# Optimization experiments

Measured on AMD Instinct MI355X. Metric: run time of the kernel, lower is better.

Reference implementation:

```python
import jax, jax.numpy as jnp
import numpy as np

HID, H, D, DFF = 128, 4, 128, 2048   # hidden_dim, nheads, out_feats per head, dim_feedforward
N, E, B = 32768, 524288, 32
EPS = 1e-5
SLOPE = 0.2  # DGL EdgeGATConv negative_slope default


def setup_inputs() -> dict:
    key = jax.random.key(0)
    ks = jax.random.split(key, 16)
    s = 0.05
    return {
        "h": jax.random.normal(ks[0], (N, HID), jnp.float32),
        "e": jax.random.normal(ks[1], (E, 1), jnp.float32),
        "src": jax.random.randint(ks[2], (E,), 0, N, jnp.int32),
        "dst": jax.random.randint(ks[3], (E,), 0, N, jnp.int32),
        "batch_size": B,
        # EdgeGATConv params (fc / fc_edge / res_fc are bias-free in DGL)
        "W_fc": jax.random.normal(ks[4], (HID, H * D), jnp.float32) * s,
        "attn_l": jax.random.normal(ks[5], (H, D), jnp.float32) * s,
        "attn_r": jax.random.normal(ks[6], (H, D), jnp.float32) * s,
        "W_fe": jax.random.normal(ks[7], (1, H * D), jnp.float32) * s,
        "attn_e": jax.random.normal(ks[8], (H, D), jnp.float32) * s,
        "W_res": jax.random.normal(ks[9], (HID, H * D), jnp.float32) * s,
        "gat_bias": jnp.zeros((H * D,), jnp.float32),
        # linear_mha + norms + FFN
        "W_mha": jax.random.normal(ks[10], (H * D, HID), jnp.float32) * s,
        "b_mha": jnp.zeros((HID,), jnp.float32),
        "n1_g": jnp.ones((HID,), jnp.float32),
        "n1_b": jnp.zeros((HID,), jnp.float32),
        "n2_g": jnp.ones((HID,), jnp.float32),
        "n2_b": jnp.zeros((HID,), jnp.float32),
        "W1": jax.random.normal(ks[11], (HID, DFF), jnp.float32) * s,
        "b1": jnp.zeros((DFF,), jnp.float32),
        "W2": jax.random.normal(ks[12], (DFF, HID), jnp.float32) * s,
        "b2": jnp.zeros((HID,), jnp.float32),
    }


def _ln(x, g, b):
    mu = x.mean(-1, keepdims=True)
    var = ((x - mu) ** 2).mean(-1, keepdims=True)
    return (x - mu) * jax.lax.rsqrt(var + EPS) * g + b


def reference(h, e, src, dst, batch_size, W_fc, attn_l, attn_r, W_fe, attn_e,
              W_res, gat_bias, W_mha, b_mha, n1_g, n1_b, n2_g, n2_b,
              W1, b1, W2, b2):
    n = h.shape[0]
    h0 = h
    # --- EdgeGATConv (eval mode: dropouts are identity) ---
    ft = (h @ W_fc).reshape(n, H, D)                         # (N,H,D)
    el = jnp.einsum("nhd,hd->nh", ft, attn_l)                # (N,H)
    er = jnp.einsum("nhd,hd->nh", ft, attn_r)
    fe = (e @ W_fe).reshape(-1, H, D)                        # (E,H,D)
    ee = jnp.einsum("ehd,hd->eh", fe, attn_e)                # (E,H)
    sc = jax.nn.leaky_relu(el[src] + er[dst] + ee, SLOPE)    # (E,H)
    # segment softmax over incoming edges of each dst node
    m = jax.ops.segment_max(sc, dst, num_segments=n)         # (N,H)
    m = jnp.where(jnp.isfinite(m), m, 0.0)                   # empty segments
    w = jnp.exp(sc - m[dst])
    z = jax.ops.segment_sum(w, dst, num_segments=n)
    zd = z[dst]
    alpha = w / jnp.where(zd == 0, 1.0, zd)                  # (E,H)
    msg = ft[src] * alpha[:, :, None]                        # (E,H,D)
    rst = jax.ops.segment_sum(msg, dst, num_segments=n)      # (N,H,D)
    rst = rst + (h0 @ W_res).reshape(n, H, D) + gat_bias.reshape(1, H, D)
    # --- transformer wrapper ---
    x = jax.nn.relu(rst).reshape(n, H * D)
    x = jax.nn.relu(x @ W_mha + b_mha)
    x = _ln(h0 + x, n1_g, n1_b)
    x = x.reshape(batch_size, -1, x.shape[1])                # (B, N/B, HID)
    ff = jax.nn.relu(x @ W1 + b1) @ W2 + b2
    return _ln(x + ff, n2_g, n2_b)
```

## Files before the change

kernel.cpp:

```cpp
#include <hip/hip_runtime.h>
#include <hip/hip_bf16.h>

#define N_NODES 32768
#define E_EDGES 524288
#define HIDDIM 128
#define FDIM 512
#define DFF 2048
#define LN_EPS 1e-5f
#define SLOPE 0.2f
#define CAP 64

typedef __bf16 bf16_t;
typedef __bf16 bf16x8 __attribute__((ext_vector_type(8)));
typedef float f32x4 __attribute__((ext_vector_type(4)));
typedef float f32x2 __attribute__((ext_vector_type(2)));

#define GLD_LDS16(gp, lp) __builtin_amdgcn_global_load_lds( \
    (const __attribute__((address_space(1))) unsigned int*)(gp), \
    (__attribute__((address_space(3))) unsigned int*)(lp), 16, 0, 0)

__device__ inline unsigned char f32_to_e4m3(float v) {
#if __has_builtin(__builtin_amdgcn_cvt_pk_fp8_f32)
    return (unsigned char)(__builtin_amdgcn_cvt_pk_fp8_f32(v, v, 0, false) & 0xff);
#else
    unsigned bits = __float_as_uint(v);
    unsigned sign = (bits >> 24) & 0x80;
    float av = fabsf(v);
    if (av >= 448.f) return (unsigned char)(sign | 0x7E);
    int e = (int)((bits >> 23) & 0xFF) - 127;
    if (e < -6) { int n = (int)rintf(av * 512.f); return (unsigned char)(sign | n); }
    float ulp = exp2f((float)(e - 3));
    int n = (int)rintf(av / ulp);
    if (n == 16) { e += 1; n = 8; }
    return (unsigned char)(sign | ((e + 7) << 3) | (n - 8));
#endif
}
template<bool HI>
__device__ inline f32x2 e4m3x2_to_f32(unsigned u) {
#if __has_builtin(__builtin_amdgcn_cvt_pk_f32_fp8)
    return __builtin_amdgcn_cvt_pk_f32_fp8(u, HI);
#else
    f32x2 r;
    unsigned b0 = HI ? ((u >> 16) & 0xff) : (u & 0xff);
    unsigned b1 = HI ? ((u >> 24) & 0xff) : ((u >> 8) & 0xff);
    unsigned bs[2] = {b0, b1};
    for (int i = 0; i < 2; ++i) {
        unsigned b = bs[i];
        float s = (b & 0x80) ? -1.f : 1.f;
        int e = (b >> 3) & 15, m = b & 7;
        float v = e ? (8 + m) * exp2f((float)(e - 10)) : m * exp2f(-9.f);
        r[i] = s * v;
    }
    return r;
#endif
}

__device__ inline void pack_range(const float* __restrict__ B, bf16_t* __restrict__ out,
                                  int id, int N) {
    const int g = id / N, n = id % N;
    union { bf16_t b[8]; uint4 u; } pk;
#pragma unroll
    for (int j = 0; j < 8; ++j) pk.b[j] = (bf16_t)B[(size_t)(g * 8 + j) * N + n];
    *(uint4*)(out + (size_t)id * 8) = pk.u;
}

__global__ __launch_bounds__(256) void prep_kernel(const float* __restrict__ h, bf16_t* __restrict__ hb,
                                                   const float* __restrict__ W_fc, bf16_t* __restrict__ Wfc_p,
                                                   const float* __restrict__ W_res, bf16_t* __restrict__ Wres_p,
                                                   const float* __restrict__ W_mha, bf16_t* __restrict__ Wmha_p,
                                                   const float* __restrict__ W1, bf16_t* __restrict__ W1_p,
                                                   const float* __restrict__ W2, bf16_t* __restrict__ W2_p,
                                                   const float* __restrict__ W_fe, const float* __restrict__ attn_e,
                                                   float* __restrict__ ce) {
    int bid = blockIdx.x;
    const int tid = threadIdx.x;
    if (bid < 4096) {
        const int id = bid * 256 + tid;
        const float4 v = ((const float4*)h)[id];
        union { bf16_t b[4]; uint2 u; } pk;
        pk.b[0] = (bf16_t)v.x; pk.b[1] = (bf16_t)v.y; pk.b[2] = (bf16_t)v.z; pk.b[3] = (bf16_t)v.w;
        *(uint2*)(hb + (size_t)id * 4) = pk.u;
        return;
    }
    bid -= 4096;
    if (bid < 32)  { pack_range(W_fc,  Wfc_p,  bid * 256 + tid, 512);  return; }
    bid -= 32;
    if (bid < 32)  { pack_range(W_res, Wres_p, bid * 256 + tid, 512);  return; }
    bid -= 32;
    if (bid < 32)  { pack_range(W_mha, Wmha_p, bid * 256 + tid, 128);  return; }
    bid -= 32;
    if (bid < 128) { pack_range(W1,    W1_p,   bid * 256 + tid, 2048); return; }
    bid -= 128;
    if (bid < 128) { pack_range(W2,    W2_p,   bid * 256 + tid, 128);  return; }
    if (tid < 128) {
        const float4 w = ((const float4*)W_fe)[tid];
        const float4 a = ((const float4*)attn_e)[tid];
        float p = w.x * a.x + w.y * a.y + w.z * a.z + w.w * a.w;
        for (int off = 16; off; off >>= 1) p += __shfl_down(p, off, 32);
        if ((tid & 31) == 0) ce[tid >> 5] = p;
    }
}

__global__ __launch_bounds__(256) void gemm_mfma(const bf16_t* __restrict__ A,
                                                 const bf16_t* __restrict__ Bp,
                                                 bf16_t* __restrict__ C,
                                                 int M, int N, int K) {
    __shared__ __align__(16) bf16_t lA[4096];
    __shared__ __align__(16) bf16_t lB[4096];
    const int tid = threadIdx.x;
    const int lane = tid & 63;
    const int wave = tid >> 6;
    const int wm = (wave >> 1) * 64, wn = (wave & 1) * 64;
    const int row0 = blockIdx.y * 128, col0 = blockIdx.x * 128;
    const int ko = lane >> 4;
    const int rl = lane & 15;
    f32x4 acc[4][4] = {};
    const int c0 = tid, c1 = tid + 256;
    const int g0 = c0 >> 7, m0 = c0 & 127;
    const int g1 = c1 >> 7, m1 = c1 & 127;
    for (int k0 = 0; k0 < K; k0 += 32) {
        __syncthreads();
        GLD_LDS16(A + (size_t)(row0 + m0) * K + k0 + g0 * 8, lA + c0 * 8);
        GLD_LDS16(A + (size_t)(row0 + m1) * K + k0 + g1 * 8, lA + c1 * 8);
        GLD_LDS16(Bp + ((size_t)(k0 / 8 + g0) * N + col0 + m0) * 8, lB + c0 * 8);
        GLD_LDS16(Bp + ((size_t)(k0 / 8 + g1) * N + col0 + m1) * 8, lB + c1 * 8);
        __syncthreads();
        bf16x8 af[4], bfr[4];
#pragma unroll
        for (int i = 0; i < 4; ++i) {
            af[i]  = *(const bf16x8*)&lA[(ko * 128 + wm + i * 16 + rl) * 8];
            bfr[i] = *(const bf16x8*)&lB[(ko * 128 + wn + i * 16 + rl) * 8];
        }
#pragma unroll
        for (int i = 0; i < 4; ++i)
#pragma unroll
            for (int j = 0; j < 4; ++j)
                acc[i][j] = __builtin_amdgcn_mfma_f32_16x16x32_bf16(af[i], bfr[j], acc[i][j], 0, 0, 0);
    }
    const int cr = (lane >> 4) * 4;
    const int cc = lane & 15;
#pragma unroll
    for (int i = 0; i < 4; ++i)
#pragma unroll
        for (int j = 0; j < 4; ++j) {
            const int col = col0 + wn + j * 16 + cc;
#pragma unroll
            for (int r = 0; r < 4; ++r) {
                const int row = row0 + wm + i * 16 + cr + r;
                C[(size_t)row * N + col] = (bf16_t)acc[i][j][r];
            }
        }
}

__global__ __launch_bounds__(256) void gemm_ft(const bf16_t* __restrict__ A,
                                               const bf16_t* __restrict__ Bp,
                                               const float* __restrict__ attn_l,
                                               const float* __restrict__ attn_r,
                                               unsigned char* __restrict__ ft8,
                                               float* __restrict__ el,
                                               float* __restrict__ er) {
    __shared__ __align__(16) bf16_t lA[4096];
    __shared__ __align__(16) bf16_t lB[4096];
    __shared__ float s_el[2][128], s_er[2][128];
    const int tid = threadIdx.x, lane = tid & 63, wave = tid >> 6;
    const int wm = (wave >> 1) * 64, wn = (wave & 1) * 64;
    const int row0 = blockIdx.y * 128;
    const int head = blockIdx.x, col0 = head * 128;
    const int ko = lane >> 4, rl = lane & 15;
    f32x4 acc[4][4] = {};
    const int c0 = tid, c1 = tid + 256;
    const int g0 = c0 >> 7, m0 = c0 & 127;
    const int g1 = c1 >> 7, m1 = c1 & 127;
    for (int k0 = 0; k0 < 128; k0 += 32) {
        __syncthreads();
        GLD_LDS16(A + (size_t)(row0 + m0) * 128 + k0 + g0 * 8, lA + c0 * 8);
        GLD_LDS16(A + (size_t)(row0 + m1) * 128 + k0 + g1 * 8, lA + c1 * 8);
        GLD_LDS16(Bp + ((size_t)(k0 / 8 + g0) * 512 + col0 + m0) * 8, lB + c0 * 8);
        GLD_LDS16(Bp + ((size_t)(k0 / 8 + g1) * 512 + col0 + m1) * 8, lB + c1 * 8);
        __syncthreads();
        bf16x8 af[4], bfr[4];
#pragma unroll
        for (int i = 0; i < 4; ++i) {
            af[i]  = *(const bf16x8*)&lA[(ko * 128 + wm + i * 16 + rl) * 8];
            bfr[i] = *(const bf16x8*)&lB[(ko * 128 + wn + i * 16 + rl) * 8];
        }
#pragma unroll
        for (int i = 0; i < 4; ++i)
#pragma unroll
            for (int j = 0; j < 4; ++j)
                acc[i][j] = __builtin_amdgcn_mfma_f32_16x16x32_bf16(af[i], bfr[j], acc[i][j], 0, 0, 0);
    }
    const int cr = (lane >> 4) * 4, cc = lane & 15;
    float al[4], ar[4];
#pragma unroll
    for (int j = 0; j < 4; ++j) {
        al[j] = attn_l[col0 + wn + j * 16 + cc];
        ar[j] = attn_r[col0 + wn + j * 16 + cc];
    }
#pragma unroll
    for (int i = 0; i < 4; ++i)
#pragma unroll
        for (int r = 0; r < 4; ++r) {
            const int row = row0 + wm + i * 16 + cr + r;
            float pel = 0.f, per = 0.f;
#pragma unroll
            for (int j = 0; j < 4; ++j) {
                const float v = acc[i][j][r];
                ft8[(size_t)row * 512 + col0 + wn + j * 16 + cc] = f32_to_e4m3(v);
                pel += v * al[j];
                per += v * ar[j];
            }
#pragma unroll
            for (int m = 1; m < 16; m <<= 1) {
                pel += __shfl_xor(pel, m);
                per += __shfl_xor(per, m);
            }
            if (cc == 0) {
                s_el[wn >> 6][wm + i * 16 + cr + r] = pel;
                s_er[wn >> 6][wm + i * 16 + cr + r] = per;
            }
        }
    __syncthreads();
    if (tid < 128) {
        el[(size_t)(row0 + tid) * 4 + head] = s_el[0][tid] + s_el[1][tid];
        er[(size_t)(row0 + tid) * 4 + head] = s_er[0][tid] + s_er[1][tid];
    }
}

__global__ __launch_bounds__(256) void gemm_mha_ln(const bf16_t* __restrict__ A,
                                                   const bf16_t* __restrict__ Bp,
                                                   const float* __restrict__ bias,
                                                   const float* __restrict__ h0,
                                                   const float* __restrict__ gamma,
                                                   const float* __restrict__ beta,
                                                   bf16_t* __restrict__ out) {
    __shared__ __align__(16) bf16_t lA[4096];
    __shared__ __align__(16) bf16_t lB[4096];
    __shared__ float s_s1[2][128], s_s2[2][128], s_mu[128], s_rs[128];
    const int tid = threadIdx.x, lane = tid & 63, wave = tid >> 6;
    const int wm = (wave >> 1) * 64, wn = (wave & 1) * 64;
    const int row0 = blockIdx.x * 128;
    const int ko = lane >> 4, rl = lane & 15;
    f32x4 acc[4][4] = {};
    const int c0 = tid, c1 = tid + 256;
    const int g0 = c0 >> 7, m0 = c0 & 127;
    const int g1 = c1 >> 7, m1 = c1 & 127;
    for (int k0 = 0; k0 < 512; k0 += 32) {
        __syncthreads();
        GLD_LDS16(A + (size_t)(row0 + m0) * 512 + k0 + g0 * 8, lA + c0 * 8);
        GLD_LDS16(A + (size_t)(row0 + m1) * 512 + k0 + g1 * 8, lA + c1 * 8);
        GLD_LDS16(Bp + ((size_t)(k0 / 8 + g0) * 128 + m0) * 8, lB + c0 * 8);
        GLD_LDS16(Bp + ((size_t)(k0 / 8 + g1) * 128 + m1) * 8, lB + c1 * 8);
        __syncthreads();
        bf16x8 af[4], bfr[4];
#pragma unroll
        for (int i = 0; i < 4; ++i) {
            af[i]  = *(const bf16x8*)&lA[(ko * 128 + wm + i * 16 + rl) * 8];
            bfr[i] = *(const bf16x8*)&lB[(ko * 128 + wn + i * 16 + rl) * 8];
        }
#pragma unroll
        for (int i = 0; i < 4; ++i)
#pragma unroll
            for (int j = 0; j < 4; ++j)
                acc[i][j] = __builtin_amdgcn_mfma_f32_16x16x32_bf16(af[i], bfr[j], acc[i][j], 0, 0, 0);
    }
    const int cr = (lane >> 4) * 4, cc = lane & 15;
#pragma unroll
    for (int j = 0; j < 4; ++j) {
        const int col = wn + j * 16 + cc;
        const float bb = bias[col];
#pragma unroll
        for (int i = 0; i < 4; ++i)
#pragma unroll
            for (int r = 0; r < 4; ++r) {
                const int row = row0 + wm + i * 16 + cr + r;
                acc[i][j][r] = fmaxf(acc[i][j][r] + bb, 0.f) + h0[(size_t)row * 128 + col];
            }
    }
#pragma unroll
    for (int i = 0; i < 4; ++i)
#pragma unroll
        for (int r = 0; r < 4; ++r) {
            float s1 = 0.f, s2 = 0.f;
#pragma unroll
            for (int j = 0; j < 4; ++j) { const float v = acc[i][j][r]; s1 += v; s2 += v * v; }
#pragma unroll
            for (int m = 1; m < 16; m <<= 1) {
                s1 += __shfl_xor(s1, m);
                s2 += __shfl_xor(s2, m);
            }
            if (cc == 0) {
                s_s1[wn >> 6][wm + i * 16 + cr + r] = s1;
                s_s2[wn >> 6][wm + i * 16 + cr + r] = s2;
            }
        }
    __syncthreads();
    if (tid < 128) {
        const float a = s_s1[0][tid] + s_s1[1][tid];
        const float q = s_s2[0][tid] + s_s2[1][tid];
        const float mu = a * (1.f / 128.f);
        s_mu[tid] = mu;
        s_rs[tid] = rsqrtf(q * (1.f / 128.f) - mu * mu + LN_EPS);
    }
    __syncthreads();
#pragma unroll
    for (int j = 0; j < 4; ++j) {
        const int col = wn + j * 16 + cc;
        const float gg = gamma[col], bb = beta[col];
#pragma unroll
        for (int i = 0; i < 4; ++i)
#pragma unroll
            for (int r = 0; r < 4; ++r) {
                const int rloc = wm + i * 16 + cr + r;
                out[(size_t)(row0 + rloc) * 128 + col] =
                    (bf16_t)((acc[i][j][r] - s_mu[rloc]) * s_rs[rloc] * gg + bb);
            }
    }
}

__global__ __launch_bounds__(256, 1) void ffn_fused(const bf16_t* __restrict__ x3,
                                                    const bf16_t* __restrict__ W1p,
                                                    const float* __restrict__ b1,
                                                    const bf16_t* __restrict__ W2p,
                                                    const float* __restrict__ b2,
                                                    const float* __restrict__ gamma,
                                                    const float* __restrict__ beta,
                                                    float* __restrict__ out) {
    __shared__ __align__(16) bf16_t lW1[2][8192];
    __shared__ __align__(16) bf16_t lW2[2][8192];
    __shared__ __align__(16) bf16_t lY[8192];
    const int tid = threadIdx.x, lane = tid & 63, wave = tid >> 6;
    const int wr = wave * 32;
    const int row0 = blockIdx.x * 128;
    const int ko = lane >> 4, rl = lane & 15;
    const int cr = ko * 4, cc = rl;

#pragma unroll
    for (int it = 0; it < 4; ++it) {
        const int c = it * 256 + tid;
        { const int g = c >> 6, n = c & 63;  GLD_LDS16(W1p + ((size_t)g * 2048 + n) * 8, lW1[0] + c * 8); }
        { const int g = c >> 7, n = c & 127; GLD_LDS16(W2p + ((size_t)g * 128 + n) * 8, lW2[0] + c * 8); }
    }
    bf16x8 afx[2][4];
#pragma unroll
    for (int i = 0; i < 2; ++i)
#pragma unroll
        for (int kk = 0; kk < 4; ++kk)
            afx[i][kk] = *(const bf16x8*)&x3[(size_t)(row0 + wr + i * 16 + rl) * 128 + (kk * 4 + ko) * 8];
    __syncthreads();

    f32x4 xacc[2][8] = {};
    for (int ch = 0; ch < 32; ++ch) {
        const int b = ch & 1;
        if (ch + 1 < 32) {
            const int nb = b ^ 1, nch = ch + 1;
#pragma unroll
            for (int it = 0; it < 4; ++it) {
                const int c = it * 256 + tid;
                { const int g = c >> 6, n = c & 63;  GLD_LDS16(W1p + ((size_t)g * 2048 + nch * 64 + n) * 8, lW1[nb] + c * 8); }
                { const int g = c >> 7, n = c & 127; GLD_LDS16(W2p + ((size_t)(nch * 8 + g) * 128 + n) * 8, lW2[nb] + c * 8); }
            }
        }
        f32x4 yacc[2][4] = {};
#pragma unroll
        for (int kk = 0; kk < 4; ++kk) {
            bf16x8 bfr[4];
#pragma unroll
            for (int j = 0; j < 4; ++j)
                bfr[j] = *(const bf16x8*)&lW1[b][((kk * 4 + ko) * 64 + j * 16 + rl) * 8];
#pragma unroll
            for (int i = 0; i < 2; ++i)
#pragma unroll
                for (int j = 0; j < 4; ++j)
                    yacc[i][j] = __builtin_amdgcn_mfma_f32_16x16x32_bf16(afx[i][kk], bfr[j], yacc[i][j], 0, 0, 0);
        }
#pragma unroll
        for (int j = 0; j < 4; ++j) {
            const int dff = j * 16 + cc;
            const float bb = b1[ch * 64 + dff];
#pragma unroll
            for (int i = 0; i < 2; ++i)
#pragma unroll
                for (int r = 0; r < 4; ++r)
                    lY[((dff >> 3) * 128 + wr + i * 16 + cr + r) * 8 + (dff & 7)] =
                        (bf16_t)fmaxf(yacc[i][j][r] + bb, 0.f);
        }
#pragma unroll
        for (int kk = 0; kk < 2; ++kk) {
            bf16x8 afY[2];
#pragma unroll
            for (int i = 0; i < 2; ++i)
                afY[i] = *(const bf16x8*)&lY[((kk * 4 + ko) * 128 + wr + i * 16 + rl) * 8];
#pragma unroll
            for (int j = 0; j < 8; ++j) {
                const bf16x8 bfr2 = *(const bf16x8*)&lW2[b][((kk * 4 + ko) * 128 + j * 16 + rl) * 8];
#pragma unroll
                for (int i = 0; i < 2; ++i)
                    xacc[i][j] = __builtin_amdgcn_mfma_f32_16x16x32_bf16(afY[i], bfr2, xacc[i][j], 0, 0, 0);
            }
        }
        __syncthreads();
    }
#pragma unroll
    for (int i = 0; i < 2; ++i)
#pragma unroll
        for (int r = 0; r < 4; ++r) {
            const int row = wr + i * 16 + cr + r;
            float s1 = 0.f, s2 = 0.f;
#pragma unroll
            for (int j = 0; j < 8; ++j) {
                const int col = j * 16 + cc;
                float v = xacc[i][j][r] + b2[col] + (float)x3[(size_t)(row0 + row) * 128 + col];
                xacc[i][j][r] = v;
                s1 += v; s2 += v * v;
            }
#pragma unroll
            for (int m = 1; m < 16; m <<= 1) {
                s1 += __shfl_xor(s1, m);
                s2 += __shfl_xor(s2, m);
            }
            const float mu = s1 * (1.f / 128.f);
            const float rs = rsqrtf(s2 * (1.f / 128.f) - mu * mu + LN_EPS);
#pragma unroll
            for (int j = 0; j < 8; ++j) {
                const int col = j * 16 + cc;
                out[(size_t)(row0 + row) * 128 + col] =
                    (xacc[i][j][r] - mu) * rs * gamma[col] + beta[col];
            }
        }
}

__global__ __launch_bounds__(256) void edge_build(const float* __restrict__ evals,
                                                  const int* __restrict__ src,
                                                  const int* __restrict__ dst,
                                                  const float* __restrict__ el,
                                                  const float* __restrict__ er,
                                                  const float* __restrict__ ce,
                                                  int* __restrict__ cursor,
                                                  int* __restrict__ csr_src,
                                                  float4* __restrict__ csr_w) {
    const int e = blockIdx.x * 256 + threadIdx.x;
    const int s = src[e], d = dst[e];
    const float ev = evals[e];
    const float4 l = *(const float4*)(el + (size_t)s * 4);
    const float4 r = *(const float4*)(er + (size_t)d * 4);
    const float4 c = *(const float4*)ce;
    float4 w;
    {
        float v;
        v = l.x + r.x + ev * c.x; v = v >= 0.f ? v : SLOPE * v; w.x = __expf(v);
        v = l.y + r.y + ev * c.y; v = v >= 0.f ? v : SLOPE * v; w.y = __expf(v);
        v = l.z + r.z + ev * c.z; v = v >= 0.f ? v : SLOPE * v; w.z = __expf(v);
        v = l.w + r.w + ev * c.w; v = v >= 0.f ? v : SLOPE * v; w.w = __expf(v);
    }
    const int pos = atomicAdd(&cursor[d], 1);
    if (pos < CAP) {
        csr_src[(size_t)d * CAP + pos] = s;
        csr_w[(size_t)d * CAP + pos] = w;
    }
}

__global__ __launch_bounds__(128) void aggregate_kernel(const unsigned char* __restrict__ ft8,
                                                        const bf16_t* __restrict__ res,
                                                        const int* __restrict__ cursor,
                                                        const int* __restrict__ csr_src,
                                                        const float4* __restrict__ csr_w,
                                                        const float* __restrict__ gat_bias,
                                                        bf16_t* __restrict__ x1) {
    const int n = blockIdx.x, t = threadIdx.x;
    __shared__ int s_src[CAP];
    __shared__ float s_w[CAP][4];
    const int deg = min(cursor[n], CAP);
    const int ht = t >> 5;
    if (t < deg) {
        s_src[t] = csr_src[(size_t)n * CAP + t];
        *(float4*)s_w[t] = csr_w[(size_t)n * CAP + t];
    }
    __syncthreads();
    float4 acc = {0.f, 0.f, 0.f, 0.f};
    float z = 0.f;
    for (int j = 0; j < deg; ++j) {
        const float w = s_w[j][ht];
        z += w;
        const unsigned u = *(const unsigned*)(ft8 + (size_t)s_src[j] * 512 + t * 4);
        const f32x2 lo = e4m3x2_to_f32<false>(u);
        const f32x2 hi = e4m3x2_to_f32<true>(u);
        acc.x += w * lo[0]; acc.y += w * lo[1];
        acc.z += w * hi[0]; acc.w += w * hi[1];
    }
    const float rz = deg > 0 ? 1.f / z : 0.f;
    const uint2 ur = *(const uint2*)(res + (size_t)n * FDIM + t * 4);
    const float4 gb = ((const float4*)gat_bias)[t];
    union { bf16_t b[4]; uint2 u; } pk;
    pk.b[0] = (bf16_t)fmaxf(acc.x * rz + __uint_as_float(ur.x << 16) + gb.x, 0.f);
    pk.b[1] = (bf16_t)fmaxf(acc.y * rz + __uint_as_float(ur.x & 0xFFFF0000u) + gb.y, 0.f);
    pk.b[2] = (bf16_t)fmaxf(acc.z * rz + __uint_as_float(ur.y << 16) + gb.z, 0.f);
    pk.b[3] = (bf16_t)fmaxf(acc.w * rz + __uint_as_float(ur.y & 0xFFFF0000u) + gb.w, 0.f);
    *(uint2*)(x1 + (size_t)n * FDIM + t * 4) = pk.u;
}

extern "C" void kernel_launch(void* const* d_in, const int* in_sizes, int n_in,
                              void* d_out, int out_size, void* d_ws, size_t ws_size,
                              hipStream_t stream) {
    const float* h        = (const float*)d_in[0];
    const float* evals    = (const float*)d_in[1];
    const int*   src      = (const int*)d_in[2];
    const int*   dst      = (const int*)d_in[3];
    const float* W_fc     = (const float*)d_in[5];
    const float* attn_l   = (const float*)d_in[6];
    const float* attn_r   = (const float*)d_in[7];
    const float* W_fe     = (const float*)d_in[8];
    const float* attn_e   = (const float*)d_in[9];
    const float* W_res    = (const float*)d_in[10];
    const float* gat_bias = (const float*)d_in[11];
    const float* W_mha    = (const float*)d_in[12];
    const float* b_mha    = (const float*)d_in[13];
    const float* n1_g     = (const float*)d_in[14];
    const float* n1_b     = (const float*)d_in[15];
    const float* n2_g     = (const float*)d_in[16];
    const float* n2_b     = (const float*)d_in[17];
    const float* W1       = (const float*)d_in[18];
    const float* b1       = (const float*)d_in[19];
    const float* W2       = (const float*)d_in[20];
    const float* b2       = (const float*)d_in[21];

    char* ws = (char*)d_ws;
    unsigned char* ft8 = (unsigned char*)(ws + 0);
    bf16_t* res     = (bf16_t*)(ws + 16777216ull);
    bf16_t* x1      = (bf16_t*)(ws + 50331648ull);
    float4* csr_w   = (float4*)(ws + 83886080ull);
    int*    csr_src = (int*)   (ws + 117440512ull);
    bf16_t* x3b     = (bf16_t*)(ws + 125829120ull);
    bf16_t* hb      = (bf16_t*)(ws + 134217728ull);
    bf16_t* Wfc_p   = (bf16_t*)(ws + 142606336ull);
    bf16_t* Wres_p  = (bf16_t*)(ws + 142737408ull);
    bf16_t* Wmha_p  = (bf16_t*)(ws + 142868480ull);
    bf16_t* W1_p    = (bf16_t*)(ws + 142999552ull);
    bf16_t* W2_p    = (bf16_t*)(ws + 143523840ull);
    float*  el      = (float*) (ws + 144048128ull);
    float*  er      = (float*) (ws + 144572416ull);
    float*  ce      = (float*) (ws + 145096704ull);
    int*    cursor  = (int*)   (ws + 145096768ull);

    if (ws_size < 146000000ull) return;

    (void)hipMemsetAsync(cursor, 0, 131072, stream);

    prep_kernel<<<4449, 256, 0, stream>>>(h, hb, W_fc, Wfc_p, W_res, Wres_p,
                                          W_mha, Wmha_p, W1, W1_p, W2, W2_p,
                                          W_fe, attn_e, ce);
    gemm_ft<<<dim3(4, 256), 256, 0, stream>>>(hb, Wfc_p, attn_l, attn_r, ft8, el, er);
    gemm_mfma<<<dim3(4, 256), 256, 0, stream>>>(hb, Wres_p, res, N_NODES, FDIM, 128);
    edge_build<<<E_EDGES / 256, 256, 0, stream>>>(evals, src, dst, el, er, ce, cursor, csr_src, csr_w);
    aggregate_kernel<<<N_NODES, 128, 0, stream>>>(ft8, res, cursor, csr_src, csr_w, gat_bias, x1);
    gemm_mha_ln<<<256, 256, 0, stream>>>(x1, Wmha_p, b_mha, h, n1_g, n1_b, x3b);
    ffn_fused<<<256, 256, 0, stream>>>(x3b, W1_p, b1, W2_p, b2, n2_g, n2_b, (float*)d_out);
}
```

Baseline: 323.7 us.

## Split FFN block across 8 waves with column groups and single-buffered weights

The fused FFN kernel moves from 4 to 8 waves per block. Waves split into row and column groups, so each wave computes half the DFF chunk columns and half the output columns. The double-buffered W1/W2 LDS staging becomes single buffering: the W2 load is issued at the start of each chunk and the next W1 chunk is prefetched while the second GEMM runs, with an extra barrier per chunk. The final LayerNorm now combines per-row partial sums from the two column groups through shared memory. The aim is more latency hiding and more waves per CU on a grid of only 256 blocks, at the cost of more synchronisation and less load/compute overlap.

```diff
diff --git a/kernel.cpp b/kernel.cpp
--- a/kernel.cpp
+++ b/kernel.cpp
@@ -318,7 +318,7 @@
     }
 }
 
-__global__ __launch_bounds__(256, 1) void ffn_fused(const bf16_t* __restrict__ x3,
+__global__ __launch_bounds__(512, 1) void ffn_fused(const bf16_t* __restrict__ x3,
                                                     const bf16_t* __restrict__ W1p,
                                                     const float* __restrict__ b1,
                                                     const bf16_t* __restrict__ W2p,
@@ -326,20 +326,21 @@
                                                     const float* __restrict__ gamma,
                                                     const float* __restrict__ beta,
                                                     float* __restrict__ out) {
-    __shared__ __align__(16) bf16_t lW1[2][8192];
-    __shared__ __align__(16) bf16_t lW2[2][8192];
+    __shared__ __align__(16) bf16_t lW1[8192];
+    __shared__ __align__(16) bf16_t lW2[8192];
     __shared__ __align__(16) bf16_t lY[8192];
+    __shared__ float s_s1[2][128], s_s2[2][128];
     const int tid = threadIdx.x, lane = tid & 63, wave = tid >> 6;
-    const int wr = wave * 32;
+    const int rg = wave >> 1, cg = wave & 1;
+    const int wr = rg * 32;
     const int row0 = blockIdx.x * 128;
     const int ko = lane >> 4, rl = lane & 15;
     const int cr = ko * 4, cc = rl;
 
 #pragma unroll
-    for (int it = 0; it < 4; ++it) {
-        const int c = it * 256 + tid;
-        { const int g = c >> 6, n = c & 63;  GLD_LDS16(W1p + ((size_t)g * 2048 + n) * 8, lW1[0] + c * 8); }
-        { const int g = c >> 7, n = c & 127; GLD_LDS16(W2p + ((size_t)g * 128 + n) * 8, lW2[0] + c * 8); }
+    for (int it = 0; it < 2; ++it) {
+        const int c = it * 512 + tid, g = c >> 6, n = c & 63;
+        GLD_LDS16(W1p + ((size_t)g * 2048 + n) * 8, lW1 + c * 8);
     }
     bf16x8 afx[2][4];
 #pragma unroll
@@ -347,36 +348,31 @@
 #pragma unroll
         for (int kk = 0; kk < 4; ++kk)
             afx[i][kk] = *(const bf16x8*)&x3[(size_t)(row0 + wr + i * 16 + rl) * 128 + (kk * 4 + ko) * 8];
-    __syncthreads();
-
-    f32x4 xacc[2][8] = {};
+
+    f32x4 xacc[2][4] = {};
     for (int ch = 0; ch < 32; ++ch) {
-        const int b = ch & 1;
-        if (ch + 1 < 32) {
-            const int nb = b ^ 1, nch = ch + 1;
-#pragma unroll
-            for (int it = 0; it < 4; ++it) {
-                const int c = it * 256 + tid;
-                { const int g = c >> 6, n = c & 63;  GLD_LDS16(W1p + ((size_t)g * 2048 + nch * 64 + n) * 8, lW1[nb] + c * 8); }
-                { const int g = c >> 7, n = c & 127; GLD_LDS16(W2p + ((size_t)(nch * 8 + g) * 128 + n) * 8, lW2[nb] + c * 8); }
-            }
-        }
-        f32x4 yacc[2][4] = {};
+        __syncthreads();
+#pragma unroll
+        for (int it = 0; it < 2; ++it) {
+            const int c = it * 512 + tid, g = c >> 7, n = c & 127;
+            GLD_LDS16(W2p + ((size_t)(ch * 8 + g) * 128 + n) * 8, lW2 + c * 8);
+        }
+        f32x4 yacc[2][2] = {};
 #pragma unroll
         for (int kk = 0; kk < 4; ++kk) {
-            bf16x8 bfr[4];
-#pragma unroll
-            for (int j = 0; j < 4; ++j)
-                bfr[j] = *(const bf16x8*)&lW1[b][((kk * 4 + ko) * 64 + j * 16 + rl) * 8];
+            bf16x8 bfr[2];
+#pragma unroll
+            for (int j = 0; j < 2; ++j)
+                bfr[j] = *(const bf16x8*)&lW1[((kk * 4 + ko) * 64 + cg * 32 + j * 16 + rl) * 8];
 #pragma unroll
             for (int i = 0; i < 2; ++i)
 #pragma unroll
-                for (int j = 0; j < 4; ++j)
+                for (int j = 0; j < 2; ++j)
                     yacc[i][j] = __builtin_amdgcn_mfma_f32_16x16x32_bf16(afx[i][kk], bfr[j], yacc[i][j], 0, 0, 0);
         }
 #pragma unroll
-        for (int j = 0; j < 4; ++j) {
-            const int dff = j * 16 + cc;
+        for (int j = 0; j < 2; ++j) {
+            const int dff = cg * 32 + j * 16 + cc;
             const float bb = b1[ch * 64 + dff];
 #pragma unroll
             for (int i = 0; i < 2; ++i)
@@ -385,21 +381,29 @@
                     lY[((dff >> 3) * 128 + wr + i * 16 + cr + r) * 8 + (dff & 7)] =
                         (bf16_t)fmaxf(yacc[i][j][r] + bb, 0.f);
         }
+        __syncthreads();
+        if (ch + 1 < 32) {
+#pragma unroll
+            for (int it = 0; it < 2; ++it) {
+                const int c = it * 512 + tid, g = c >> 6, n = c & 63;
+                GLD_LDS16(W1p + ((size_t)g * 2048 + (ch + 1) * 64 + n) * 8, lW1 + c * 8);
+            }
+        }
 #pragma unroll
         for (int kk = 0; kk < 2; ++kk) {
-            bf16x8 afY[2];
+            bf16x8 afY[2], bfr2[4];
 #pragma unroll
             for (int i = 0; i < 2; ++i)
                 afY[i] = *(const bf16x8*)&lY[((kk * 4 + ko) * 128 + wr + i * 16 + rl) * 8];
 #pragma unroll
-            for (int j = 0; j < 8; ++j) {
-                const bf16x8 bfr2 = *(const bf16x8*)&lW2[b][((kk * 4 + ko) * 128 + j * 16 + rl) * 8];
-#pragma unroll
-                for (int i = 0; i < 2; ++i)
-                    xacc[i][j] = __builtin_amdgcn_mfma_f32_16x16x32_bf16(afY[i], bfr2, xacc[i][j], 0, 0, 0);
-            }
-        }
-        __syncthreads();
+            for (int j = 0; j < 4; ++j)
+                bfr2[j] = *(const bf16x8*)&lW2[((kk * 4 + ko) * 128 + cg * 64 + j * 16 + rl) * 8];
+#pragma unroll
+            for (int i = 0; i < 2; ++i)
+#pragma unroll
+                for (int j = 0; j < 4; ++j)
+                    xacc[i][j] = __builtin_amdgcn_mfma_f32_16x16x32_bf16(afY[i], bfr2[j], xacc[i][j], 0, 0, 0);
+        }
     }
 #pragma unroll
     for (int i = 0; i < 2; ++i)
@@ -408,8 +412,8 @@
             const int row = wr + i * 16 + cr + r;
             float s1 = 0.f, s2 = 0.f;
 #pragma unroll
-            for (int j = 0; j < 8; ++j) {
-                const int col = j * 16 + cc;
+            for (int j = 0; j < 4; ++j) {
+                const int col = cg * 64 + j * 16 + cc;
                 float v = xacc[i][j][r] + b2[col] + (float)x3[(size_t)(row0 + row) * 128 + col];
                 xacc[i][j][r] = v;
                 s1 += v; s2 += v * v;
@@ -419,11 +423,21 @@
                 s1 += __shfl_xor(s1, m);
                 s2 += __shfl_xor(s2, m);
             }
-            const float mu = s1 * (1.f / 128.f);
-            const float rs = rsqrtf(s2 * (1.f / 128.f) - mu * mu + LN_EPS);
-#pragma unroll
-            for (int j = 0; j < 8; ++j) {
-                const int col = j * 16 + cc;
+            if (cc == 0) { s_s1[cg][row] = s1; s_s2[cg][row] = s2; }
+        }
+    __syncthreads();
+#pragma unroll
+    for (int i = 0; i < 2; ++i)
+#pragma unroll
+        for (int r = 0; r < 4; ++r) {
+            const int row = wr + i * 16 + cr + r;
+            const float a = s_s1[0][row] + s_s1[1][row];
+            const float q = s_s2[0][row] + s_s2[1][row];
+            const float mu = a * (1.f / 128.f);
+            const float rs = rsqrtf(q * (1.f / 128.f) - mu * mu + LN_EPS);
+#pragma unroll
+            for (int j = 0; j < 4; ++j) {
+                const int col = cg * 64 + j * 16 + cc;
                 out[(size_t)(row0 + row) * 128 + col] =
                     (xacc[i][j][r] - mu) * rs * gamma[col] + beta[col];
             }
@@ -554,5 +568,5 @@
     edge_build<<<E_EDGES / 256, 256, 0, stream>>>(evals, src, dst, el, er, ce, cursor, csr_src, csr_w);
     aggregate_kernel<<<N_NODES, 128, 0, stream>>>(ft8, res, cursor, csr_src, csr_w, gat_bias, x1);
     gemm_mha_ln<<<256, 256, 0, stream>>>(x1, Wmha_p, b_mha, h, n1_g, n1_b, x3b);
-    ffn_fused<<<256, 256, 0, stream>>>(x3b, W1_p, b1, W2_p, b2, n2_g, n2_b, (float*)d_out);
-}
+    ffn_fused<<<256, 512, 0, stream>>>(x3b, W1_p, b1, W2_p, b2, n2_g, n2_b, (float*)d_out);
+}
```

Result: faster. 300.2 us (-7.3%).
